# Kernel optimization log

Hardware: AMD Instinct MI355X
Metric: run time of the kernel (lower is better)

The kernel has to match this reference:

```python
import jax, jax.numpy as jnp
import numpy as np

N_BITS_W = 8      # weight quant bits
N_BITS_A = 8      # activation quant bits
SCALE_RANGE_IN = 1.0
BN_EPS = 1e-5
ACT_THRES = 6.0   # ReLUN clamp


def _fake_quant(v, n_bits, scaling_range):
    """Symmetric uniform fake-quantization with straight-through estimator.
    Layer-wise scale from the max-abs value (Qmodes.layer_wise)."""
    qp = float(2 ** (n_bits - 1) - 1)
    alpha = scaling_range * jnp.max(jnp.abs(v))
    step = alpha / qp
    q = jnp.clip(jnp.round(v / step), -qp, qp) * step
    # STE: forward uses q, gradient flows through v unchanged
    return v + jax.lax.stop_gradient(q - v)


def setup_inputs() -> dict:
    key = jax.random.key(0)
    k1, k2 = jax.random.split(key)
    x = jax.random.normal(k1, (32, 16, 224, 224), dtype=jnp.float32)
    # Kaiming-ish scale for a 3x3 conv with 16 in-channels
    weight = jax.random.normal(k2, (16, 16, 3, 3), dtype=jnp.float32) * (1.0 / np.sqrt(16 * 9))
    gamma = jnp.ones((16,), dtype=jnp.float32)
    beta = jnp.zeros((16,), dtype=jnp.float32)
    return {"x": x, "weight": weight, "gamma": gamma, "beta": beta}


def reference(x, weight, gamma, beta):
    # --- GemmConv2d with quant_flag=True, noise_flag=False ---
    xq = _fake_quant(x, N_BITS_A, SCALE_RANGE_IN)
    wq = _fake_quant(weight, N_BITS_W, 1.0)
    y = jax.lax.conv_general_dilated(
        xq, wq,
        window_strides=(1, 1),
        padding=[(1, 1), (1, 1)],
        dimension_numbers=("NCHW", "OIHW", "NCHW"),
    )  # [N, Cout, H, W]
    # --- BatchNorm2d (training mode: batch statistics, biased variance) ---
    mean = jnp.mean(y, axis=(0, 2, 3))
    var = jnp.var(y, axis=(0, 2, 3))
    inv = gamma * jax.lax.rsqrt(var + BN_EPS)
    y = y * inv[None, :, None, None] + (beta - mean * inv)[None, :, None, None]
    # --- ReLUN(6): clamp to [0, act_thres] ---
    return jnp.clip(y, 0.0, ACT_THRES)
```

## Files before the change

### kernel.cpp

```cpp
#include <hip/hip_runtime.h>
#include <stdint.h>

#define QP 127.0f
#define HW2 50176
#define NPIX 1605632
#define NELEM 25690112
#define ABS_GRID 2048
#define NRG 56
#define NBLK_CONV 1792

#define WS_WQ    256
#define WS_BMAX  4096
#define WS_PART  16384
#define WS_XQ    (1 << 20)

__device__ __forceinline__ int dot4(int a, int b, int c) {
#if defined(__has_builtin) && __has_builtin(__builtin_amdgcn_sdot4)
  return __builtin_amdgcn_sdot4(a, b, c, false);
#else
  int r = c;
  r += (int)(signed char)(a)       * (int)(signed char)(b);
  r += (int)(signed char)(a >> 8)  * (int)(signed char)(b >> 8);
  r += (int)(signed char)(a >> 16) * (int)(signed char)(b >> 16);
  r += (a >> 24) * (b >> 24);
  return r;
#endif
}

__device__ __forceinline__ void conv_strip(const int4* sXs, const int4* wq4,
                                           int cx, int (&acc)[4][16]) {
  #pragma unroll 1
  for (int kw = 0; kw < 3; ++kw) {
    int4 xr[6];
    #pragma unroll
    for (int j = 0; j < 6; ++j) xr[j] = sXs[j * 226 + cx + kw];
    #pragma unroll
    for (int c = 0; c < 16; ++c) {
      #pragma unroll
      for (int kh = 0; kh < 3; ++kh) {
        int4 wv = wq4[(c * 3 + kh) * 3 + kw];
        #pragma unroll
        for (int p = 0; p < 4; ++p) {
          int4 xv = xr[p + kh];
          int a = acc[p][c];
          a = dot4(xv.x, wv.x, a);
          a = dot4(xv.y, wv.y, a);
          a = dot4(xv.z, wv.z, a);
          a = dot4(xv.w, wv.w, a);
          acc[p][c] = a;
        }
      }
    }
  }
}

__device__ __forceinline__ void stage_strip(const int4* __restrict__ xq,
                                            int4* sXs, int n, int r0, int tid) {
  #pragma unroll
  for (int j = 0; j < 6; ++j) {
    int g = r0 - 1 + j;
    if (tid < 224) {
      int4 v = {0, 0, 0, 0};
      if ((unsigned)g < 224u) v = xq[(n * 224 + g) * 224 + tid];
      sXs[j * 226 + 1 + tid] = v;
    } else if (tid < 226) {
      int4 z = {0, 0, 0, 0};
      sXs[j * 226 + ((tid == 224) ? 0 : 225)] = z;
    }
  }
}

__global__ __launch_bounds__(256) void k_absmax_wq(const float* __restrict__ x,
                                                   const float* __restrict__ w,
                                                   char* __restrict__ ws) {
  __shared__ float red[4];
  __shared__ float s_sw;
  float* hdr_f = (float*)ws;
  float* bmax = (float*)(ws + WS_BMAX);
  int* wq = (int*)(ws + WS_WQ);
  const int tid = threadIdx.x;

  const float4* x4 = (const float4*)x;
  float m = 0.0f;
  for (int i = blockIdx.x * 256 + tid; i < NELEM / 4; i += ABS_GRID * 256) {
    float4 v = x4[i];
    m = fmaxf(m, fmaxf(fmaxf(fabsf(v.x), fabsf(v.y)),
                       fmaxf(fabsf(v.z), fabsf(v.w))));
  }
  #pragma unroll
  for (int off = 32; off; off >>= 1) m = fmaxf(m, __shfl_down(m, off, 64));
  if ((tid & 63) == 0) red[tid >> 6] = m;
  __syncthreads();
  if (tid == 0)
    bmax[blockIdx.x] = fmaxf(fmaxf(red[0], red[1]), fmaxf(red[2], red[3]));

  if (blockIdx.x == 0) {
    __syncthreads();
    float mw = 0.0f;
    for (int i = tid; i < 2304; i += 256) mw = fmaxf(mw, fabsf(w[i]));
    #pragma unroll
    for (int off = 32; off; off >>= 1) mw = fmaxf(mw, __shfl_down(mw, off, 64));
    if ((tid & 63) == 0) red[tid >> 6] = mw;
    __syncthreads();
    if (tid == 0) {
      float sw = fmaxf(fmaxf(red[0], red[1]), fmaxf(red[2], red[3])) / QP;
      hdr_f[1] = sw;
      s_sw = sw;
    }
    __syncthreads();
    float sw = s_sw;
    for (int i = tid; i < 576; i += 256) {
      int cout = i / 36; int r = i - cout * 36;
      int tap = r >> 2;  int c4 = r & 3;
      int kh = tap / 3, kw = tap - kh * 3;
      unsigned bits = 0;
      #pragma unroll
      for (int j = 0; j < 4; ++j) {
        int cin = c4 * 4 + j;
        float v = w[((cout * 16 + cin) * 3 + kh) * 3 + kw];
        int q = (int)rintf(v / sw);
        q = max(-127, min(127, q));
        bits |= ((unsigned)(q & 0xff)) << (8 * j);
      }
      wq[i] = (int)bits;
    }
  }
}

__global__ __launch_bounds__(256) void k_quant_x(const float* __restrict__ x,
                                                 char* __restrict__ ws) {
  __shared__ float sRed4[4];
  const float* __restrict__ bmax = (const float*)(ws + WS_BMAX);
  float* hdr_f = (float*)ws;
  int4* xq = (int4*)(ws + WS_XQ);
  const int tid = threadIdx.x;

  float m = 0.0f;
  for (int i = tid; i < ABS_GRID; i += 256) m = fmaxf(m, bmax[i]);
  #pragma unroll
  for (int off = 32; off; off >>= 1) m = fmaxf(m, __shfl_down(m, off, 64));
  if ((tid & 63) == 0) sRed4[tid >> 6] = m;
  __syncthreads();
  const float sx =
      fmaxf(fmaxf(sRed4[0], sRed4[1]), fmaxf(sRed4[2], sRed4[3])) / QP;
  if (blockIdx.x == 0 && tid == 0) hdr_f[2] = sx;

  int t = blockIdx.x * 256 + tid;
  int p0 = t * 4;
  int n = p0 / HW2;
  int hw = p0 - n * HW2;
  const float4* xb = (const float4*)(x + (size_t)n * 16 * HW2 + hw);
  unsigned comp[4][4];
  #pragma unroll
  for (int j = 0; j < 4; ++j)
    #pragma unroll
    for (int k = 0; k < 4; ++k) comp[j][k] = 0u;
  #pragma unroll
  for (int c = 0; c < 16; ++c) {
    float4 vc = xb[c * (HW2 / 4)];
    float f[4] = {vc.x, vc.y, vc.z, vc.w};
    #pragma unroll
    for (int j = 0; j < 4; ++j) {
      int q = (int)rintf(f[j] / sx);
      q = max(-127, min(127, q));
      comp[j][c >> 2] |= ((unsigned)(q & 0xff)) << (8 * (c & 3));
    }
  }
  #pragma unroll
  for (int j = 0; j < 4; ++j) {
    int4 v;
    v.x = (int)comp[j][0]; v.y = (int)comp[j][1];
    v.z = (int)comp[j][2]; v.w = (int)comp[j][3];
    xq[p0 + j] = v;
  }
}

__global__ __launch_bounds__(256) void k_conv_stats(const char* __restrict__ ws,
                                                    float* __restrict__ partials) {
  __shared__ int4 sXs[6 * 226];
  __shared__ float sRedS[4][16];
  __shared__ float sRedQ[4][16];
  const int4* __restrict__ xq = (const int4*)(ws + WS_XQ);
  const int4* __restrict__ wq4 = (const int4*)(ws + WS_WQ);

  const int tid = threadIdx.x;
  const int b = blockIdx.x;
  const int n = b / NRG, rg = b - n * NRG;
  const int r0 = rg * 4;

  stage_strip(xq, sXs, n, r0, tid);
  __syncthreads();

  int acc[4][16];
  #pragma unroll
  for (int p = 0; p < 4; ++p)
    #pragma unroll
    for (int c = 0; c < 16; ++c) acc[p][c] = 0;
  if (tid < 224) conv_strip(sXs, wq4, tid, acc);

  float* sR = (float*)sXs;
  int wv_ = tid >> 6, cc = tid & 15;
  const int colbase = (tid >> 4) << 4;
  __syncthreads();
  #pragma unroll
  for (int c = 0; c < 16; ++c) {
    int si = acc[0][c] + acc[1][c] + acc[2][c] + acc[3][c];
    sR[c * 257 + tid] = (float)si;
  }
  __syncthreads();
  {
    float ps = 0.0f;
    #pragma unroll
    for (int j = 0; j < 16; ++j) ps += sR[cc * 257 + colbase + j];
    ps += __shfl_xor(ps, 16, 64);
    ps += __shfl_xor(ps, 32, 64);
    if ((tid & 63) < 16) sRedS[wv_][cc] = ps;
  }
  __syncthreads();
  #pragma unroll
  for (int c = 0; c < 16; ++c) {
    float f0 = (float)acc[0][c], f1 = (float)acc[1][c];
    float f2 = (float)acc[2][c], f3 = (float)acc[3][c];
    sR[c * 257 + tid] = f0 * f0 + f1 * f1 + f2 * f2 + f3 * f3;
  }
  __syncthreads();
  {
    float pq = 0.0f;
    #pragma unroll
    for (int j = 0; j < 16; ++j) pq += sR[cc * 257 + colbase + j];
    pq += __shfl_xor(pq, 16, 64);
    pq += __shfl_xor(pq, 32, 64);
    if ((tid & 63) < 16) sRedQ[wv_][cc] = pq;
  }
  __syncthreads();
  if (tid < 32) {
    int c = tid & 15;
    float t;
    if (tid < 16) t = sRedS[0][c] + sRedS[1][c] + sRedS[2][c] + sRedS[3][c];
    else          t = sRedQ[0][c] + sRedQ[1][c] + sRedQ[2][c] + sRedQ[3][c];
    partials[b * 32 + tid] = t;
  }
}

__global__ void k_finalize(const float* __restrict__ partials,
                           const float* __restrict__ gamma,
                           const float* __restrict__ beta,
                           float* __restrict__ hdr_f) {
  __shared__ double sdd[256][4];
  __shared__ double sfin[32];
  int t = threadIdx.x;
  const float4* p4 = (const float4*)partials;
  double d0 = 0, d1 = 0, d2 = 0, d3 = 0;
  #pragma unroll 8
  for (int k = 0; k < 56; ++k) {
    float4 v = p4[t + 256 * k];
    d0 += (double)v.x; d1 += (double)v.y; d2 += (double)v.z; d3 += (double)v.w;
  }
  sdd[t][0] = d0; sdd[t][1] = d1; sdd[t][2] = d2; sdd[t][3] = d3;
  __syncthreads();
  if (t < 32) {
    double s = 0.0;
    #pragma unroll 8
    for (int i = 0; i < 32; ++i) s += sdd[(t >> 2) + 8 * i][t & 3];
    sfin[t] = s;
  }
  __syncthreads();
  if (t < 16) {
    float sf = hdr_f[2] * hdr_f[1];
    double s = (double)sf;
    const double M = (double)NPIX;
    double mean = s * sfin[t] / M;
    double ey2 = s * s * sfin[16 + t] / M;
    double var = ey2 - mean * mean;
    double inv = (double)gamma[t] / sqrt(var + 1e-5);
    hdr_f[16 + t] = (float)(s * inv);
    hdr_f[32 + t] = (float)((double)beta[t] - mean * inv);
  }
}

__global__ __launch_bounds__(256) void k_conv_out(const char* __restrict__ ws,
                                                  float* __restrict__ out) {
  __shared__ int4 sXs[6 * 226];
  const int4* __restrict__ xq = (const int4*)(ws + WS_XQ);
  const int4* __restrict__ wq4 = (const int4*)(ws + WS_WQ);
  const float* hdr_f = (const float*)ws;

  const int tid = threadIdx.x;
  const int b = blockIdx.x;
  const int n = b / NRG, rg = b - n * NRG;
  const int r0 = rg * 4;

  stage_strip(xq, sXs, n, r0, tid);
  __syncthreads();

  if (tid < 224) {
    int acc[4][16];
    #pragma unroll
    for (int p = 0; p < 4; ++p)
      #pragma unroll
      for (int c = 0; c < 16; ++c) acc[p][c] = 0;
    conv_strip(sXs, wq4, tid, acc);

    #pragma unroll
    for (int c = 0; c < 16; ++c) {
      float A = hdr_f[16 + c], B = hdr_f[32 + c];
      #pragma unroll
      for (int p = 0; p < 4; ++p) {
        float y = fmaf((float)acc[p][c], A, B);
        y = fminf(fmaxf(y, 0.0f), 6.0f);
        out[((n * 16 + c) * 224 + (r0 + p)) * 224 + tid] = y;
      }
    }
  }
}

extern "C" void kernel_launch(void* const* d_in, const int* in_sizes, int n_in,
                              void* d_out, int out_size, void* d_ws, size_t ws_size,
                              hipStream_t stream) {
  const float* x = (const float*)d_in[0];
  const float* w = (const float*)d_in[1];
  const float* gamma = (const float*)d_in[2];
  const float* beta = (const float*)d_in[3];
  float* out = (float*)d_out;
  char* ws = (char*)d_ws;
  float* partials = (float*)(ws + WS_PART);

  k_absmax_wq<<<ABS_GRID, 256, 0, stream>>>(x, w, ws);
  k_quant_x<<<1568, 256, 0, stream>>>(x, ws);
  k_conv_stats<<<NBLK_CONV, 256, 0, stream>>>(ws, partials);
  k_finalize<<<1, 256, 0, stream>>>(partials, gamma, beta, (float*)ws);
  k_conv_out<<<NBLK_CONV, 256, 0, stream>>>(ws, out);
}
```

Before: 283.0 us.

## Fuse all stages into one cooperative persistent kernel with grid syncs

Replaces the five-kernel pipeline with a single cooperative kernel that uses grid-wide syncs between the absmax, the fused quantize+conv-stats pass, the BN finalize, and the conv-output pass. Quantization of x is folded into the stats pass, so the separate quant kernel and its extra read of x are gone. The grid is sized from occupancy, with a fallback to the old launches. This removes launch gaps and one full pass over the input, at the cost of grid-sync overhead and a persistent grid that may cap parallelism below the old launch sizes.

```diff
diff --git a/kernel.cpp b/kernel.cpp
--- a/kernel.cpp
+++ b/kernel.cpp
@@ -1,5 +1,8 @@
 #include <hip/hip_runtime.h>
+#include <hip/hip_cooperative_groups.h>
 #include <stdint.h>
+
+namespace cg = cooperative_groups;
 
 #define QP 127.0f
 #define HW2 50176
@@ -70,6 +73,251 @@
   }
 }
 
+__global__ __launch_bounds__(256) void k_mega(
+    const float* __restrict__ x, const float* __restrict__ w,
+    const float* __restrict__ gamma, const float* __restrict__ beta,
+    float* __restrict__ out, char* __restrict__ ws) {
+  __shared__ int4 sXs[6 * 226];
+  __shared__ float sRedS[4][16];
+  __shared__ float sRedQ[4][16];
+  __shared__ float sRed4[4];
+  __shared__ float s_sw;
+
+  float* hdr_f = (float*)ws;
+  int* wqd = (int*)(ws + WS_WQ);
+  const int4* wq4 = (const int4*)(ws + WS_WQ);
+  float* bmax = (float*)(ws + WS_BMAX);
+  float* partials = (float*)(ws + WS_PART);
+  int4* xq = (int4*)(ws + WS_XQ);
+
+  const int tid = threadIdx.x;
+  const int G = gridDim.x;
+
+  {
+    const float4* x4 = (const float4*)x;
+    float m = 0.0f;
+    for (int i = blockIdx.x * 256 + tid; i < NELEM / 4; i += G * 256) {
+      float4 v = x4[i];
+      m = fmaxf(m, fmaxf(fmaxf(fabsf(v.x), fabsf(v.y)),
+                         fmaxf(fabsf(v.z), fabsf(v.w))));
+    }
+    #pragma unroll
+    for (int off = 32; off; off >>= 1) m = fmaxf(m, __shfl_down(m, off, 64));
+    if ((tid & 63) == 0) sRed4[tid >> 6] = m;
+    __syncthreads();
+    if (tid == 0)
+      bmax[blockIdx.x] =
+          fmaxf(fmaxf(sRed4[0], sRed4[1]), fmaxf(sRed4[2], sRed4[3]));
+
+    if (blockIdx.x == 0) {
+      __syncthreads();
+      float mw = 0.0f;
+      for (int i = tid; i < 2304; i += 256) mw = fmaxf(mw, fabsf(w[i]));
+      #pragma unroll
+      for (int off = 32; off; off >>= 1) mw = fmaxf(mw, __shfl_down(mw, off, 64));
+      if ((tid & 63) == 0) sRed4[tid >> 6] = mw;
+      __syncthreads();
+      if (tid == 0) {
+        float sw = fmaxf(fmaxf(sRed4[0], sRed4[1]), fmaxf(sRed4[2], sRed4[3])) / QP;
+        hdr_f[1] = sw;
+        s_sw = sw;
+      }
+      __syncthreads();
+      float sw = s_sw;
+      for (int i = tid; i < 576; i += 256) {
+        int cout = i / 36; int r = i - cout * 36;
+        int tap = r >> 2;  int c4 = r & 3;
+        int kh = tap / 3, kw2 = tap - kh * 3;
+        unsigned bits = 0;
+        #pragma unroll
+        for (int j = 0; j < 4; ++j) {
+          int cin = c4 * 4 + j;
+          float v = w[((cout * 16 + cin) * 3 + kh) * 3 + kw2];
+          int q = (int)rintf(v / sw);
+          q = max(-127, min(127, q));
+          bits |= ((unsigned)(q & 0xff)) << (8 * j);
+        }
+        wqd[i] = (int)bits;
+      }
+    }
+  }
+  cg::this_grid().sync();
+
+  __syncthreads();
+  float m2 = 0.0f;
+  for (int i = tid; i < G; i += 256) m2 = fmaxf(m2, bmax[i]);
+  #pragma unroll
+  for (int off = 32; off; off >>= 1) m2 = fmaxf(m2, __shfl_down(m2, off, 64));
+  if ((tid & 63) == 0) sRed4[tid >> 6] = m2;
+  __syncthreads();
+  const float sx =
+      fmaxf(fmaxf(sRed4[0], sRed4[1]), fmaxf(sRed4[2], sRed4[3])) / QP;
+
+  for (int strip = blockIdx.x; strip < NBLK_CONV; strip += G) {
+    const int n = strip / NRG, rg = strip - n * NRG;
+    const int r0 = rg * 4;
+
+    for (int task = tid; task < 336; task += 256) {
+      int j = task / 56, g = task - j * 56;
+      int gr = r0 - 1 + j;
+      int4 v[4] = {{0,0,0,0}, {0,0,0,0}, {0,0,0,0}, {0,0,0,0}};
+      if ((unsigned)gr < 224u) {
+        const float4* xb = (const float4*)x + (size_t)n * 16 * (HW2 / 4)
+                           + gr * 56 + g;
+        unsigned comp[4][4];
+        #pragma unroll
+        for (int k = 0; k < 4; ++k)
+          #pragma unroll
+          for (int q4 = 0; q4 < 4; ++q4) comp[k][q4] = 0u;
+        #pragma unroll
+        for (int c = 0; c < 16; ++c) {
+          float4 vc = xb[c * (HW2 / 4)];
+          float f[4] = {vc.x, vc.y, vc.z, vc.w};
+          #pragma unroll
+          for (int k = 0; k < 4; ++k) {
+            int q = (int)rintf(f[k] / sx);
+            q = max(-127, min(127, q));
+            comp[k][c >> 2] |= ((unsigned)(q & 0xff)) << (8 * (c & 3));
+          }
+        }
+        #pragma unroll
+        for (int k = 0; k < 4; ++k) {
+          v[k].x = (int)comp[k][0]; v[k].y = (int)comp[k][1];
+          v[k].z = (int)comp[k][2]; v[k].w = (int)comp[k][3];
+        }
+        if (j >= 1 && j <= 4) {
+          #pragma unroll
+          for (int k = 0; k < 4; ++k)
+            xq[(n * 224 + gr) * 224 + 4 * g + k] = v[k];
+        }
+      }
+      #pragma unroll
+      for (int k = 0; k < 4; ++k) sXs[j * 226 + 1 + 4 * g + k] = v[k];
+    }
+    if (tid >= 244) {
+      int idx = tid - 244;
+      int4 z = {0, 0, 0, 0};
+      sXs[(idx >> 1) * 226 + ((idx & 1) ? 225 : 0)] = z;
+    }
+    __syncthreads();
+
+    int acc[4][16];
+    #pragma unroll
+    for (int p = 0; p < 4; ++p)
+      #pragma unroll
+      for (int c = 0; c < 16; ++c) acc[p][c] = 0;
+    if (tid < 224) conv_strip(sXs, wq4, tid, acc);
+
+    float* sR = (float*)sXs;
+    int wv_ = tid >> 6, cc = tid & 15;
+    const int colbase = (tid >> 4) << 4;
+    __syncthreads();
+    #pragma unroll
+    for (int c = 0; c < 16; ++c) {
+      int si = acc[0][c] + acc[1][c] + acc[2][c] + acc[3][c];
+      sR[c * 257 + tid] = (float)si;
+    }
+    __syncthreads();
+    {
+      float ps = 0.0f;
+      #pragma unroll
+      for (int j = 0; j < 16; ++j) ps += sR[cc * 257 + colbase + j];
+      ps += __shfl_xor(ps, 16, 64);
+      ps += __shfl_xor(ps, 32, 64);
+      if ((tid & 63) < 16) sRedS[wv_][cc] = ps;
+    }
+    __syncthreads();
+    #pragma unroll
+    for (int c = 0; c < 16; ++c) {
+      float f0 = (float)acc[0][c], f1 = (float)acc[1][c];
+      float f2 = (float)acc[2][c], f3 = (float)acc[3][c];
+      sR[c * 257 + tid] = f0 * f0 + f1 * f1 + f2 * f2 + f3 * f3;
+    }
+    __syncthreads();
+    {
+      float pq = 0.0f;
+      #pragma unroll
+      for (int j = 0; j < 16; ++j) pq += sR[cc * 257 + colbase + j];
+      pq += __shfl_xor(pq, 16, 64);
+      pq += __shfl_xor(pq, 32, 64);
+      if ((tid & 63) < 16) sRedQ[wv_][cc] = pq;
+    }
+    __syncthreads();
+    if (tid < 32) {
+      int c = tid & 15;
+      float t;
+      if (tid < 16) t = sRedS[0][c] + sRedS[1][c] + sRedS[2][c] + sRedS[3][c];
+      else          t = sRedQ[0][c] + sRedQ[1][c] + sRedQ[2][c] + sRedQ[3][c];
+      partials[strip * 32 + tid] = t;
+    }
+    __syncthreads();
+  }
+  cg::this_grid().sync();
+
+  if (blockIdx.x == 0) {
+    double* sdd = (double*)sXs;
+    double* sfin = ((double*)sXs) + 1024;
+    const float4* p4 = (const float4*)partials;
+    double d0 = 0, d1 = 0, d2 = 0, d3 = 0;
+    #pragma unroll 8
+    for (int k = 0; k < 56; ++k) {
+      float4 v = p4[tid + 256 * k];
+      d0 += (double)v.x; d1 += (double)v.y; d2 += (double)v.z; d3 += (double)v.w;
+    }
+    sdd[tid * 4 + 0] = d0; sdd[tid * 4 + 1] = d1;
+    sdd[tid * 4 + 2] = d2; sdd[tid * 4 + 3] = d3;
+    __syncthreads();
+    if (tid < 32) {
+      double s = 0.0;
+      #pragma unroll 8
+      for (int i = 0; i < 32; ++i) s += sdd[((tid >> 2) + 8 * i) * 4 + (tid & 3)];
+      sfin[tid] = s;
+    }
+    __syncthreads();
+    if (tid < 16) {
+      float sf = sx * hdr_f[1];
+      double s = (double)sf;
+      const double M = (double)NPIX;
+      double mean = s * sfin[tid] / M;
+      double ey2 = s * s * sfin[16 + tid] / M;
+      double var = ey2 - mean * mean;
+      double inv = (double)gamma[tid] / sqrt(var + 1e-5);
+      hdr_f[16 + tid] = (float)(s * inv);
+      hdr_f[32 + tid] = (float)((double)beta[tid] - mean * inv);
+    }
+  }
+  cg::this_grid().sync();
+
+  for (int strip = blockIdx.x; strip < NBLK_CONV; strip += G) {
+    const int n = strip / NRG, rg = strip - n * NRG;
+    const int r0 = rg * 4;
+
+    stage_strip(xq, sXs, n, r0, tid);
+    __syncthreads();
+
+    if (tid < 224) {
+      int acc[4][16];
+      #pragma unroll
+      for (int p = 0; p < 4; ++p)
+        #pragma unroll
+        for (int c = 0; c < 16; ++c) acc[p][c] = 0;
+      conv_strip(sXs, wq4, tid, acc);
+
+      #pragma unroll
+      for (int c = 0; c < 16; ++c) {
+        float A = hdr_f[16 + c], B = hdr_f[32 + c];
+        #pragma unroll
+        for (int p = 0; p < 4; ++p) {
+          float y = fmaf((float)acc[p][c], A, B);
+          y = fminf(fmaxf(y, 0.0f), 6.0f);
+          out[((n * 16 + c) * 224 + (r0 + p)) * 224 + tid] = y;
+        }
+      }
+    }
+    __syncthreads();
+  }
+}
+
 __global__ __launch_bounds__(256) void k_absmax_wq(const float* __restrict__ x,
                                                    const float* __restrict__ w,
                                                    char* __restrict__ ws) {
@@ -325,9 +573,39 @@
   char* ws = (char*)d_ws;
   float* partials = (float*)(ws + WS_PART);
 
-  k_absmax_wq<<<ABS_GRID, 256, 0, stream>>>(x, w, ws);
-  k_quant_x<<<1568, 256, 0, stream>>>(x, ws);
-  k_conv_stats<<<NBLK_CONV, 256, 0, stream>>>(ws, partials);
-  k_finalize<<<1, 256, 0, stream>>>(partials, gamma, beta, (float*)ws);
-  k_conv_out<<<NBLK_CONV, 256, 0, stream>>>(ws, out);
-}
+  static int s_grid = 0;
+  if (s_grid == 0) {
+    int occ = 0;
+    hipError_t e = hipOccupancyMaxActiveBlocksPerMultiprocessor(&occ, k_mega, 256, 0);
+    if (e != hipSuccess || occ < 1) {
+      s_grid = -1;
+      (void)hipGetLastError();
+    } else {
+      int g = occ * 256;
+      if (g > NBLK_CONV) g = NBLK_CONV;
+      s_grid = g;
+    }
+  }
+
+  bool done = false;
+  if (s_grid > 0) {
+    void* args[] = {(void*)&x, (void*)&w, (void*)&gamma, (void*)&beta,
+                    (void*)&out, (void*)&ws};
+    hipError_t e = hipLaunchCooperativeKernel(k_mega, dim3(s_grid), dim3(256),
+                                              args, 0u, stream);
+    if (e == hipSuccess) {
+      done = true;
+    } else {
+      s_grid = -1;
+      (void)hipGetLastError();
+    }
+  }
+
+  if (!done) {
+    k_absmax_wq<<<ABS_GRID, 256, 0, stream>>>(x, w, ws);
+    k_quant_x<<<1568, 256, 0, stream>>>(x, ws);
+    k_conv_stats<<<NBLK_CONV, 256, 0, stream>>>(ws, partials);
+    k_finalize<<<1, 256, 0, stream>>>(partials, gamma, beta, (float*)ws);
+    k_conv_out<<<NBLK_CONV, 256, 0, stream>>>(ws, out);
+  }
+}
```

After: 551.4 us. 1.95x slower.

## Compute int8 conv with MFMA 16x16x64 instead of scalar sdot4 loops

Applied to the files above, without the earlier changes.

Replaces the per-thread sdot4 convolution in both the stats and output kernels with MFMA i32_16x16x64_i8 instructions. Each wave computes 16-pixel by 16-channel tiles, with the 9 taps times 16 channels packed as a K of 192 (three MFMAs, last chunk zero-padded). The stats reduction is simplified to per-lane accumulation plus shuffles, dropping several shared-memory passes and barriers. Output stores become float4 per lane. Risks include MFMA operand layout correctness and the wasted padded K.

```diff
diff --git a/kernel.cpp b/kernel.cpp
--- a/kernel.cpp
+++ b/kernel.cpp
@@ -14,45 +14,7 @@
 #define WS_PART  16384
 #define WS_XQ    (1 << 20)
 
-__device__ __forceinline__ int dot4(int a, int b, int c) {
-#if defined(__has_builtin) && __has_builtin(__builtin_amdgcn_sdot4)
-  return __builtin_amdgcn_sdot4(a, b, c, false);
-#else
-  int r = c;
-  r += (int)(signed char)(a)       * (int)(signed char)(b);
-  r += (int)(signed char)(a >> 8)  * (int)(signed char)(b >> 8);
-  r += (int)(signed char)(a >> 16) * (int)(signed char)(b >> 16);
-  r += (a >> 24) * (b >> 24);
-  return r;
-#endif
-}
-
-__device__ __forceinline__ void conv_strip(const int4* sXs, const int4* wq4,
-                                           int cx, int (&acc)[4][16]) {
-  #pragma unroll 1
-  for (int kw = 0; kw < 3; ++kw) {
-    int4 xr[6];
-    #pragma unroll
-    for (int j = 0; j < 6; ++j) xr[j] = sXs[j * 226 + cx + kw];
-    #pragma unroll
-    for (int c = 0; c < 16; ++c) {
-      #pragma unroll
-      for (int kh = 0; kh < 3; ++kh) {
-        int4 wv = wq4[(c * 3 + kh) * 3 + kw];
-        #pragma unroll
-        for (int p = 0; p < 4; ++p) {
-          int4 xv = xr[p + kh];
-          int a = acc[p][c];
-          a = dot4(xv.x, wv.x, a);
-          a = dot4(xv.y, wv.y, a);
-          a = dot4(xv.z, wv.z, a);
-          a = dot4(xv.w, wv.w, a);
-          acc[p][c] = a;
-        }
-      }
-    }
-  }
-}
+typedef int v4i __attribute__((ext_vector_type(4)));
 
 __device__ __forceinline__ void stage_strip(const int4* __restrict__ xq,
                                             int4* sXs, int n, int r0, int tid) {
@@ -67,6 +29,24 @@
       int4 z = {0, 0, 0, 0};
       sXs[j * 226 + ((tid == 224) ? 0 : 225)] = z;
     }
+  }
+}
+
+__device__ __forceinline__ void conv_lane_setup(const int4* __restrict__ wq4,
+                                                int ccol, int chunk,
+                                                v4i (&bfrag)[3], int (&abase)[3]) {
+  #pragma unroll
+  for (int m = 0; m < 3; ++m) {
+    int tap = 4 * m + chunk;
+    v4i bv = {0, 0, 0, 0};
+    if (tap <= 8) {
+      int4 t = wq4[ccol * 9 + tap];
+      bv[0] = t.x; bv[1] = t.y; bv[2] = t.z; bv[3] = t.w;
+    }
+    bfrag[m] = bv;
+    int tc = (tap > 8) ? 8 : tap;
+    int kh = tc / 3, kw = tc - kh * 3;
+    abase[m] = kh * 226 + ccol + kw;
   }
 }
 
@@ -178,8 +158,8 @@
 __global__ __launch_bounds__(256) void k_conv_stats(const char* __restrict__ ws,
                                                     float* __restrict__ partials) {
   __shared__ int4 sXs[6 * 226];
-  __shared__ float sRedS[4][16];
-  __shared__ float sRedQ[4][16];
+  __shared__ int   sS[4][16];
+  __shared__ float sQ[4][16];
   const int4* __restrict__ xq = (const int4*)(ws + WS_XQ);
   const int4* __restrict__ wq4 = (const int4*)(ws + WS_WQ);
 
@@ -189,55 +169,45 @@
   const int r0 = rg * 4;
 
   stage_strip(xq, sXs, n, r0, tid);
-  __syncthreads();
-
-  int acc[4][16];
-  #pragma unroll
-  for (int p = 0; p < 4; ++p)
-    #pragma unroll
-    for (int c = 0; c < 16; ++c) acc[p][c] = 0;
-  if (tid < 224) conv_strip(sXs, wq4, tid, acc);
-
-  float* sR = (float*)sXs;
-  int wv_ = tid >> 6, cc = tid & 15;
-  const int colbase = (tid >> 4) << 4;
-  __syncthreads();
-  #pragma unroll
-  for (int c = 0; c < 16; ++c) {
-    int si = acc[0][c] + acc[1][c] + acc[2][c] + acc[3][c];
-    sR[c * 257 + tid] = (float)si;
-  }
-  __syncthreads();
-  {
-    float ps = 0.0f;
-    #pragma unroll
-    for (int j = 0; j < 16; ++j) ps += sR[cc * 257 + colbase + j];
-    ps += __shfl_xor(ps, 16, 64);
-    ps += __shfl_xor(ps, 32, 64);
-    if ((tid & 63) < 16) sRedS[wv_][cc] = ps;
-  }
-  __syncthreads();
-  #pragma unroll
-  for (int c = 0; c < 16; ++c) {
-    float f0 = (float)acc[0][c], f1 = (float)acc[1][c];
-    float f2 = (float)acc[2][c], f3 = (float)acc[3][c];
-    sR[c * 257 + tid] = f0 * f0 + f1 * f1 + f2 * f2 + f3 * f3;
-  }
-  __syncthreads();
-  {
-    float pq = 0.0f;
-    #pragma unroll
-    for (int j = 0; j < 16; ++j) pq += sR[cc * 257 + colbase + j];
-    pq += __shfl_xor(pq, 16, 64);
-    pq += __shfl_xor(pq, 32, 64);
-    if ((tid & 63) < 16) sRedQ[wv_][cc] = pq;
-  }
+
+  const int lane = tid & 63, wid = tid >> 6;
+  const int ccol = lane & 15, chunk = lane >> 4;
+  v4i bfrag[3];
+  int abase[3];
+  conv_lane_setup(wq4, ccol, chunk, bfrag, abase);
+  __syncthreads();
+
+  int   sAcc = 0;
+  float qAcc = 0.0f;
+  for (int t = wid; t < 56; t += 4) {
+    int ty = t / 14, x0 = (t - ty * 14) << 4;
+    int off = ty * 226 + x0;
+    v4i acc = {0, 0, 0, 0};
+    #pragma unroll
+    for (int m = 0; m < 3; ++m) {
+      int4 av = sXs[off + abase[m]];
+      v4i a; a[0] = av.x; a[1] = av.y; a[2] = av.z; a[3] = av.w;
+      acc = __builtin_amdgcn_mfma_i32_16x16x64_i8(a, bfrag[m], acc, 0, 0, 0);
+    }
+    #pragma unroll
+    for (int r = 0; r < 4; ++r) {
+      int d = acc[r];
+      sAcc += d;
+      float f = (float)d;
+      qAcc += f * f;
+    }
+  }
+  sAcc += __shfl_xor(sAcc, 16, 64);
+  sAcc += __shfl_xor(sAcc, 32, 64);
+  qAcc += __shfl_xor(qAcc, 16, 64);
+  qAcc += __shfl_xor(qAcc, 32, 64);
+  if (lane < 16) { sS[wid][ccol] = sAcc; sQ[wid][ccol] = qAcc; }
   __syncthreads();
   if (tid < 32) {
     int c = tid & 15;
     float t;
-    if (tid < 16) t = sRedS[0][c] + sRedS[1][c] + sRedS[2][c] + sRedS[3][c];
-    else          t = sRedQ[0][c] + sRedQ[1][c] + sRedQ[2][c] + sRedQ[3][c];
+    if (tid < 16) t = (float)(sS[0][c] + sS[1][c] + sS[2][c] + sS[3][c]);
+    else          t = sQ[0][c] + sQ[1][c] + sQ[2][c] + sQ[3][c];
     partials[b * 32 + tid] = t;
   }
 }
@@ -291,26 +261,35 @@
   const int r0 = rg * 4;
 
   stage_strip(xq, sXs, n, r0, tid);
-  __syncthreads();
-
-  if (tid < 224) {
-    int acc[4][16];
-    #pragma unroll
-    for (int p = 0; p < 4; ++p)
-      #pragma unroll
-      for (int c = 0; c < 16; ++c) acc[p][c] = 0;
-    conv_strip(sXs, wq4, tid, acc);
-
-    #pragma unroll
-    for (int c = 0; c < 16; ++c) {
-      float A = hdr_f[16 + c], B = hdr_f[32 + c];
-      #pragma unroll
-      for (int p = 0; p < 4; ++p) {
-        float y = fmaf((float)acc[p][c], A, B);
-        y = fminf(fmaxf(y, 0.0f), 6.0f);
-        out[((n * 16 + c) * 224 + (r0 + p)) * 224 + tid] = y;
-      }
-    }
+
+  const int lane = tid & 63, wid = tid >> 6;
+  const int ccol = lane & 15, chunk = lane >> 4;
+  v4i bfrag[3];
+  int abase[3];
+  conv_lane_setup(wq4, ccol, chunk, bfrag, abase);
+  const float Af = hdr_f[16 + ccol];
+  const float Bf = hdr_f[32 + ccol];
+  __syncthreads();
+
+  float* oplane = out + ((size_t)n * 16 + ccol) * HW2;
+  for (int t = wid; t < 56; t += 4) {
+    int ty = t / 14, x0 = (t - ty * 14) << 4;
+    int off = ty * 226 + x0;
+    v4i acc = {0, 0, 0, 0};
+    #pragma unroll
+    for (int m = 0; m < 3; ++m) {
+      int4 av = sXs[off + abase[m]];
+      v4i a; a[0] = av.x; a[1] = av.y; a[2] = av.z; a[3] = av.w;
+      acc = __builtin_amdgcn_mfma_i32_16x16x64_i8(a, bfrag[m], acc, 0, 0, 0);
+    }
+    float4 o;
+    float v0 = fminf(fmaxf(fmaf((float)acc[0], Af, Bf), 0.0f), 6.0f);
+    float v1 = fminf(fmaxf(fmaf((float)acc[1], Af, Bf), 0.0f), 6.0f);
+    float v2 = fminf(fmaxf(fmaf((float)acc[2], Af, Bf), 0.0f), 6.0f);
+    float v3 = fminf(fmaxf(fmaf((float)acc[3], Af, Bf), 0.0f), 6.0f);
+    o.x = v0; o.y = v1; o.z = v2; o.w = v3;
+    int y = r0 + ty, xb = x0 + chunk * 4;
+    *(float4*)&oplane[y * 224 + xb] = o;
   }
 }
 
```

After: 239.5 us. 1.18x faster.
